# Performance work log

Measured on AMD Instinct MI355X. Metric: run time of the kernel, lower is better.

## Reference

```python
import jax, jax.numpy as jnp
import numpy as np

FEATS = 768
HEAD = 12


def _phi(t):
    # elu feature map + 1 (guarantees positivity)
    return jax.nn.elu(t) + 1.0


def setup_inputs() -> dict:
    key = jax.random.key(0)
    ks = jax.random.split(key, 9)
    f = FEATS
    s = 1.0 / np.sqrt(f)
    x = jax.random.normal(ks[0], (4, 4096, f), dtype=jnp.float32)
    # weights stored as [in, out] so projection is x @ W + b
    Wq = jax.random.normal(ks[1], (f, f), dtype=jnp.float32) * s
    bq = jax.random.normal(ks[2], (f,), dtype=jnp.float32) * 0.01
    Wk = jax.random.normal(ks[3], (f, f), dtype=jnp.float32) * s
    bk = jax.random.normal(ks[4], (f,), dtype=jnp.float32) * 0.01
    Wv = jax.random.normal(ks[5], (f, f), dtype=jnp.float32) * s
    bv = jax.random.normal(ks[6], (f,), dtype=jnp.float32) * 0.01
    Wo = jax.random.normal(ks[7], (f, f), dtype=jnp.float32) * s
    bo = jax.random.normal(ks[8], (f,), dtype=jnp.float32) * 0.01
    return {"x": x, "Wq": Wq, "bq": bq, "Wk": Wk, "bk": bk,
            "Wv": Wv, "bv": bv, "Wo": Wo, "bo": bo}


def reference(x, Wq, bq, Wk, bk, Wv, bv, Wo, bo):
    b, n, f = x.shape
    h = HEAD
    d = f // h
    # project and split heads: [b, h, n, d]
    def heads(t):
        return t.reshape(b, n, h, d).transpose(0, 2, 1, 3)
    q = _phi(heads(x @ Wq + bq))
    k = _phi(heads(x @ Wk + bk))
    v = heads(x @ Wv + bv)
    # kv summary: [b, h, d, d] (sum over sequence)
    kv = jnp.einsum('bhnd,bhne->bhde', k, v)
    # normalizer: z[b,h,l] = 1 / (q[b,h,l,:] . sum_n k[b,h,n,:])  (no eps, as in source)
    ksum = k.sum(axis=2)                      # [b, h, d]
    z = 1.0 / jnp.einsum('bhld,bhd->bhl', q, ksum)  # [b, h, n]
    num = jnp.einsum('bhld,bhde->bhle', q, kv)      # [b, h, n, d]
    normed = num * z[..., None]                     # [b, h, n, d]
    out = normed.transpose(0, 2, 1, 3).reshape(b, n, f)  # [b, n, f]
    return out @ Wo + bo  # dropout p=0.0 -> identity
```

## Files before the change

kernel.cpp:

```cpp
#include <hip/hip_runtime.h>
#include <cstdint>
#include <cstddef>

#define DEVI __device__ __forceinline__

typedef short    shortx8 __attribute__((ext_vector_type(8)));
typedef short    shortx4 __attribute__((ext_vector_type(4)));
typedef short    shortx2 __attribute__((ext_vector_type(2)));
typedef __bf16   bf16x8  __attribute__((ext_vector_type(8)));
typedef float    floatx4 __attribute__((ext_vector_type(4)));

DEVI unsigned short f2b(float f) {
    union { float f; unsigned u; } a; a.f = f;
    unsigned r = a.u + 0x7fffu + ((a.u >> 16) & 1u);
    return (unsigned short)(r >> 16);
}
DEVI float b2f(unsigned short u) {
    union { unsigned u; float f; } a; a.u = ((unsigned)u) << 16;
    return a.f;
}

DEVI floatx4 mfma_bf16(bf16x8 a, bf16x8 b, floatx4 c) {
    return __builtin_amdgcn_mfma_f32_16x16x32_bf16(a, b, c, 0, 0, 0);
}

DEVI void glds16(const ushort* g, ushort* l) {
    __builtin_amdgcn_global_load_lds(
        (const __attribute__((address_space(1))) void*)g,
        (__attribute__((address_space(3))) void*)l, 16, 0, 0);
}

__global__ void k_prep(const float* __restrict__ x, ushort* __restrict__ xb,
                       const float* __restrict__ Wq, const float* __restrict__ Wk,
                       const float* __restrict__ Wv, const float* __restrict__ Wo,
                       ushort* __restrict__ Wt, ushort* __restrict__ Wot,
                       const float* __restrict__ bq, const float* __restrict__ bk,
                       const float* __restrict__ bv, float* __restrict__ bqkv) {
    __shared__ float tile[64][65];
    const int bid = blockIdx.x, t = threadIdx.x;
    if (bid < 6144) {
        size_t i = ((size_t)bid * 256 + t) * 8;
        float4 v0 = *(const float4*)(x + i);
        float4 v1 = *(const float4*)(x + i + 4);
        shortx8 o;
        o[0] = (short)f2b(v0.x); o[1] = (short)f2b(v0.y);
        o[2] = (short)f2b(v0.z); o[3] = (short)f2b(v0.w);
        o[4] = (short)f2b(v1.x); o[5] = (short)f2b(v1.y);
        o[6] = (short)f2b(v1.z); o[7] = (short)f2b(v1.w);
        *(shortx8*)(xb + i) = o;
    } else if (bid < 6720) {
        int pid = bid - 6144;
        int zi = pid / 144, rem = pid % 144;
        const float* W = (zi == 0) ? Wq : (zi == 1) ? Wk : (zi == 2) ? Wv : Wo;
        const int i0 = (rem / 12) * 64, j0 = (rem % 12) * 64;
        const int c = t & 63, r4 = t >> 6;
        for (int rr = r4; rr < 64; rr += 4)
            tile[rr][c] = W[(size_t)(i0 + rr) * 768 + j0 + c];
        __syncthreads();
        ushort* dst = (zi < 3) ? (Wt + (size_t)(zi * 768) * 768) : Wot;
        for (int jj = r4; jj < 64; jj += 4)
            dst[(size_t)(j0 + jj) * 768 + i0 + c] = f2b(tile[c][jj]);
    } else {
        int j = (bid - 6720) * 256 + t;
        if (j < 2304) {
            const float* src = (j < 768) ? bq : (j < 1536) ? bk : bv;
            bqkv[j] = src[j % 768];
        }
    }
}

template <int MODE>
__global__ __launch_bounds__(256, 2) void k_gemm(
    const ushort* __restrict__ A, const ushort* __restrict__ Bt,
    const float* __restrict__ bias, void* __restrict__ Cout, int Ncols) {
    constexpr int K = 768;
    __shared__ ushort As[128 * 64];
    __shared__ ushort Bs[128 * 64];
    const int m0 = blockIdx.x * 128;
    const int n0 = blockIdx.y * 128;
    const int tid = threadIdx.x;
    const int w = tid >> 6, lane = tid & 63;

    const int lr = lane >> 3;
    const int lc = ((lane & 7) ^ lr) * 8;
    const ushort* ag[4]; const ushort* bg[4]; ushort* al[4]; ushort* bl[4];
#pragma unroll
    for (int i = 0; i < 4; ++i) {
        ag[i] = A  + (size_t)(m0 + w * 32 + i * 8 + lr) * K + lc;
        bg[i] = Bt + (size_t)(n0 + w * 32 + i * 8 + lr) * K + lc;
        al[i] = As + (w * 32 + i * 8) * 64;
        bl[i] = Bs + (w * 32 + i * 8) * 64;
    }

    const int rBase = (w >> 1) * 64;
    const int nBase = (w & 1) * 64;
    const int fr = lane & 15;
    const int q4 = lane >> 4;

    floatx4 acc[4][4] = {};

    for (int k0 = 0; k0 < K; k0 += 64) {
#pragma unroll
        for (int i = 0; i < 4; ++i) glds16(ag[i] + k0, al[i]);
#pragma unroll
        for (int i = 0; i < 4; ++i) glds16(bg[i] + k0, bl[i]);
        __syncthreads();
#pragma unroll
        for (int kc = 0; kc < 2; ++kc) {
            const int off = ((kc * 4 + q4) ^ (fr & 7)) * 8;
            bf16x8 af[4], bf[4];
#pragma unroll
            for (int rt = 0; rt < 4; ++rt)
                af[rt] = *(const bf16x8*)(As + (rBase + rt * 16 + fr) * 64 + off);
#pragma unroll
            for (int nt = 0; nt < 4; ++nt)
                bf[nt] = *(const bf16x8*)(Bs + (nBase + nt * 16 + fr) * 64 + off);
#pragma unroll
            for (int rt = 0; rt < 4; ++rt)
#pragma unroll
                for (int nt = 0; nt < 4; ++nt)
                    acc[rt][nt] = mfma_bf16(af[rt], bf[nt], acc[rt][nt]);
        }
        __syncthreads();
    }

#pragma unroll
    for (int rt = 0; rt < 4; ++rt) {
#pragma unroll
        for (int nt = 0; nt < 4; ++nt) {
#pragma unroll
            for (int r = 0; r < 4; ++r) {
                int m = m0 + rBase + rt * 16 + q4 * 4 + r;
                int n = n0 + nBase + nt * 16 + fr;
                float v = acc[rt][nt][r] + bias[n];
                if (MODE == 0) {
                    if (n < 1536) v = (v > 0.f) ? (v + 1.f) : __expf(v);
                    ((ushort*)Cout)[(size_t)m * Ncols + n] = f2b(v);
                } else {
                    ((float*)Cout)[(size_t)m * Ncols + n] = v;
                }
            }
        }
    }
}

__global__ __launch_bounds__(256) void k_kv(const ushort* __restrict__ QKV,
                                            float* __restrict__ kvp) {
    const int bh = blockIdx.x, s = blockIdx.y;
    const int bb = bh / 12, head = bh % 12;
    __shared__ ushort kS[64 * 70];
    __shared__ ushort vS[64 * 70];
    const int t = threadIdx.x, w = t >> 6, lane = t & 63;
    const int fr = lane & 15, fk = (lane >> 4) * 8;

    floatx4 acc[5] = {};
    const int n_ld = t >> 2, c16 = (t & 3) * 16;
    const ushort* base = QKV + (size_t)(bb * 4096 + s * 512) * 2304 + 768 + head * 64 + c16;

    for (int rr = 0; rr < 8; ++rr) {
        if (rr) __syncthreads();
        {
            const ushort* kp = base + (size_t)(rr * 64 + n_ld) * 2304;
            union { shortx8 v8; shortx2 v2[4]; } k0, k1, v0, v1;
            k0.v8 = *(const shortx8*)(kp);
            k1.v8 = *(const shortx8*)(kp + 8);
            v0.v8 = *(const shortx8*)(kp + 768);
            v1.v8 = *(const shortx8*)(kp + 776);
            ushort* kd = kS + n_ld * 70 + c16;
            ushort* vd = vS + n_ld * 70 + c16;
#pragma unroll
            for (int i = 0; i < 4; ++i) {
                *(shortx2*)(kd + 2 * i)     = k0.v2[i];
                *(shortx2*)(kd + 8 + 2 * i) = k1.v2[i];
                *(shortx2*)(vd + 2 * i)     = v0.v2[i];
                *(shortx2*)(vd + 8 + 2 * i) = v1.v2[i];
            }
        }
        __syncthreads();
#pragma unroll
        for (int kl = 0; kl < 64; kl += 32) {
            union { bf16x8 v; ushort u[8]; } bfr, afr[4];
#pragma unroll
            for (int i = 0; i < 8; ++i) {
                int n = kl + fk + i;
                bfr.u[i] = kS[n * 70 + w * 16 + fr];
#pragma unroll
                for (int mt = 0; mt < 4; ++mt)
                    afr[mt].u[i] = vS[n * 70 + mt * 16 + fr];
            }
            union { bf16x8 v; ushort u[8]; } ones;
            ushort ov = (fr == 0) ? (ushort)0x3F80 : (ushort)0;
#pragma unroll
            for (int i = 0; i < 8; ++i) ones.u[i] = ov;
#pragma unroll
            for (int mt = 0; mt < 4; ++mt)
                acc[mt] = mfma_bf16(afr[mt].v, bfr.v, acc[mt]);
            acc[4] = mfma_bf16(ones.v, bfr.v, acc[4]);
        }
    }

    float* dst = kvp + ((size_t)bh * 8 + s) * (65 * 64);
#pragma unroll
    for (int mt = 0; mt < 4; ++mt)
#pragma unroll
        for (int r = 0; r < 4; ++r)
            dst[(mt * 16 + (lane >> 4) * 4 + r) * 64 + w * 16 + fr] = acc[mt][r];
    if (lane < 16) dst[64 * 64 + w * 16 + lane] = acc[4][0];
}

__global__ void k_kvred(const float* __restrict__ kvp, ushort* __restrict__ kvb) {
    int t4 = (blockIdx.x * 256 + threadIdx.x) * 4;
    int bh = t4 / 4160, rem = t4 % 4160;
    const float* p = kvp + (size_t)bh * 8 * 4160 + rem;
    float4 sum = {0.f, 0.f, 0.f, 0.f};
    for (int i = 0; i < 8; ++i) {
        float4 a = *(const float4*)(p + (size_t)i * 4160);
        sum.x += a.x; sum.y += a.y; sum.z += a.z; sum.w += a.w;
    }
    shortx4 o;
    o[0] = (short)f2b(sum.x); o[1] = (short)f2b(sum.y);
    o[2] = (short)f2b(sum.z); o[3] = (short)f2b(sum.w);
    *(shortx4*)(kvb + t4) = o;
}

__global__ __launch_bounds__(256) void k_num(const ushort* __restrict__ QKV,
                                             const ushort* __restrict__ kvb,
                                             ushort* __restrict__ normed) {
    const int bh = blockIdx.x, l0 = blockIdx.y * 128;
    const int bb = bh / 12, head = bh % 12;
    __shared__ ushort qsh[128 * 72];
    __shared__ ushort kvT[80 * 72];
    __shared__ float dnm[128];
    const int t = threadIdx.x, w = t >> 6, lane = t & 63;

    {
        const ushort* kvbb = kvb + (size_t)bh * 4160;
        int c8 = (t & 7) * 8;
        for (int r0 = (t >> 3); r0 < 65; r0 += 32)
            *(shortx8*)(kvT + r0 * 72 + c8) = *(const shortx8*)(kvbb + r0 * 64 + c8);
    }
    for (int idx = t; idx < 15 * 72; idx += 256) kvT[65 * 72 + idx] = 0;

    const ushort* qg = QKV + (size_t)(bb * 4096 + l0) * 2304 + head * 64;
    {
        int row = t >> 3, c8 = (t & 7) * 8;
#pragma unroll
        for (int i = 0; i < 4; ++i) {
            shortx8 v = *(const shortx8*)(qg + (size_t)(i * 32 + row) * 2304 + c8);
            *(shortx8*)(qsh + (i * 32 + row) * 72 + c8) = v;
        }
    }
    __syncthreads();

    const int fr = lane & 15, fk = (lane >> 4) * 8;
    floatx4 acc[2][5] = {};
#pragma unroll
    for (int kc = 0; kc < 2; ++kc) {
        bf16x8 a[2], b[5];
#pragma unroll
        for (int rt = 0; rt < 2; ++rt)
            a[rt] = *(const bf16x8*)(qsh + (w * 32 + rt * 16 + fr) * 72 + kc * 32 + fk);
#pragma unroll
        for (int nt = 0; nt < 5; ++nt)
            b[nt] = *(const bf16x8*)(kvT + (nt * 16 + fr) * 72 + kc * 32 + fk);
#pragma unroll
        for (int rt = 0; rt < 2; ++rt)
#pragma unroll
            for (int nt = 0; nt < 5; ++nt)
                acc[rt][nt] = mfma_bf16(a[rt], b[nt], acc[rt][nt]);
    }
    if (fr == 0) {
#pragma unroll
        for (int rt = 0; rt < 2; ++rt)
#pragma unroll
            for (int r = 0; r < 4; ++r)
                dnm[w * 32 + rt * 16 + (lane >> 4) * 4 + r] = acc[rt][4][r];
    }
    __syncthreads();
#pragma unroll
    for (int rt = 0; rt < 2; ++rt) {
#pragma unroll
        for (int r = 0; r < 4; ++r) {
            int ml = w * 32 + rt * 16 + (lane >> 4) * 4 + r;
            float z = 1.f / dnm[ml];
            size_t base = (size_t)(bb * 4096 + l0 + ml) * 768 + head * 64;
#pragma unroll
            for (int nt = 0; nt < 4; ++nt)
                normed[base + nt * 16 + fr] = f2b(acc[rt][nt][r] * z);
        }
    }
}

extern "C" void kernel_launch(void* const* d_in, const int* in_sizes, int n_in,
                              void* d_out, int out_size, void* d_ws, size_t ws_size,
                              hipStream_t stream) {
    const float* x  = (const float*)d_in[0];
    const float* Wq = (const float*)d_in[1];
    const float* bq = (const float*)d_in[2];
    const float* Wk = (const float*)d_in[3];
    const float* bk = (const float*)d_in[4];
    const float* Wv = (const float*)d_in[5];
    const float* bv = (const float*)d_in[6];
    const float* Wo = (const float*)d_in[7];
    const float* bo = (const float*)d_in[8];

    char* ws = (char*)d_ws;
    ushort* Xb   = (ushort*)(ws);
    ushort* Wt   = (ushort*)(ws + 25165824);
    ushort* Wot  = (ushort*)(ws + 28704768);
    float*  bqkv = (float*)(ws + 29884416);
    ushort* QKV  = (ushort*)(ws + 29893632);
    float*  kvp  = (float*)(ws + 105391104);
    ushort* kvb  = (ushort*)(ws + 111780864);
    ushort* normed = Xb;

    k_prep <<<dim3(6729),      256, 0, stream>>>(x, Xb, Wq, Wk, Wv, Wo, Wt, Wot,
                                                 bq, bk, bv, bqkv);
    k_gemm<0><<<dim3(128, 18), 256, 0, stream>>>(Xb, Wt, bqkv, (void*)QKV, 2304);
    k_kv   <<<dim3(48, 8),     256, 0, stream>>>(QKV, kvp);
    k_kvred<<<dim3(195),       256, 0, stream>>>(kvp, kvb);
    k_num  <<<dim3(48, 32),    256, 0, stream>>>(QKV, kvb, normed);
    k_gemm<1><<<dim3(128, 6),  256, 0, stream>>>(normed, Wot, bo, d_out, 768);
}
```

Measured before the change: 237.8 us.

## Load GEMM B operand directly to registers and stage normed output through LDS

The GEMM kernel stops staging the weight tile in shared memory. Each wave loads its B fragments straight from global memory into registers, which halves LDS use, and launch bounds are raised to three blocks per CU for more occupancy. The attention kernel now writes its normalized output into shared memory first and then stores it to global with coalesced 16-byte writes instead of scattered 2-byte stores. The risks are that the B loads from global are now duplicated across waves and less coalesced, and that register pressure rises under the tighter launch bound.

Result: slower. 313.6 us (+31.8%).

```diff
diff --git a/kernel.cpp b/kernel.cpp
--- a/kernel.cpp
+++ b/kernel.cpp
@@ -70,12 +70,11 @@
 }
 
 template <int MODE>
-__global__ __launch_bounds__(256, 2) void k_gemm(
+__global__ __launch_bounds__(256, 3) void k_gemm(
     const ushort* __restrict__ A, const ushort* __restrict__ Bt,
     const float* __restrict__ bias, void* __restrict__ Cout, int Ncols) {
     constexpr int K = 768;
     __shared__ ushort As[128 * 64];
-    __shared__ ushort Bs[128 * 64];
     const int m0 = blockIdx.x * 128;
     const int n0 = blockIdx.y * 128;
     const int tid = threadIdx.x;
@@ -83,13 +82,11 @@
 
     const int lr = lane >> 3;
     const int lc = ((lane & 7) ^ lr) * 8;
-    const ushort* ag[4]; const ushort* bg[4]; ushort* al[4]; ushort* bl[4];
+    const ushort* ag[4]; ushort* al[4];
 #pragma unroll
     for (int i = 0; i < 4; ++i) {
-        ag[i] = A  + (size_t)(m0 + w * 32 + i * 8 + lr) * K + lc;
-        bg[i] = Bt + (size_t)(n0 + w * 32 + i * 8 + lr) * K + lc;
+        ag[i] = A + (size_t)(m0 + w * 32 + i * 8 + lr) * K + lc;
         al[i] = As + (w * 32 + i * 8) * 64;
-        bl[i] = Bs + (w * 32 + i * 8) * 64;
     }
 
     const int rBase = (w >> 1) * 64;
@@ -97,29 +94,35 @@
     const int fr = lane & 15;
     const int q4 = lane >> 4;
 
+    const ushort* bp[4];
+#pragma unroll
+    for (int nt = 0; nt < 4; ++nt)
+        bp[nt] = Bt + (size_t)(n0 + nBase + nt * 16 + fr) * K + q4 * 8;
+
     floatx4 acc[4][4] = {};
 
     for (int k0 = 0; k0 < K; k0 += 64) {
 #pragma unroll
         for (int i = 0; i < 4; ++i) glds16(ag[i] + k0, al[i]);
-#pragma unroll
-        for (int i = 0; i < 4; ++i) glds16(bg[i] + k0, bl[i]);
+        bf16x8 bf[2][4];
+#pragma unroll
+        for (int kc = 0; kc < 2; ++kc)
+#pragma unroll
+            for (int nt = 0; nt < 4; ++nt)
+                bf[kc][nt] = *(const bf16x8*)(bp[nt] + k0 + kc * 32);
         __syncthreads();
 #pragma unroll
         for (int kc = 0; kc < 2; ++kc) {
             const int off = ((kc * 4 + q4) ^ (fr & 7)) * 8;
-            bf16x8 af[4], bf[4];
+            bf16x8 af[4];
 #pragma unroll
             for (int rt = 0; rt < 4; ++rt)
                 af[rt] = *(const bf16x8*)(As + (rBase + rt * 16 + fr) * 64 + off);
 #pragma unroll
-            for (int nt = 0; nt < 4; ++nt)
-                bf[nt] = *(const bf16x8*)(Bs + (nBase + nt * 16 + fr) * 64 + off);
-#pragma unroll
             for (int rt = 0; rt < 4; ++rt)
 #pragma unroll
                 for (int nt = 0; nt < 4; ++nt)
-                    acc[rt][nt] = mfma_bf16(af[rt], bf[nt], acc[rt][nt]);
+                    acc[rt][nt] = mfma_bf16(af[rt], bf[kc][nt], acc[rt][nt]);
         }
         __syncthreads();
     }
@@ -277,16 +280,27 @@
                 dnm[w * 32 + rt * 16 + (lane >> 4) * 4 + r] = acc[rt][4][r];
     }
     __syncthreads();
+
+    ushort* osh = qsh;
 #pragma unroll
     for (int rt = 0; rt < 2; ++rt) {
 #pragma unroll
         for (int r = 0; r < 4; ++r) {
             int ml = w * 32 + rt * 16 + (lane >> 4) * 4 + r;
             float z = 1.f / dnm[ml];
-            size_t base = (size_t)(bb * 4096 + l0 + ml) * 768 + head * 64;
 #pragma unroll
             for (int nt = 0; nt < 4; ++nt)
-                normed[base + nt * 16 + fr] = f2b(acc[rt][nt][r] * z);
+                osh[ml * 72 + nt * 16 + fr] = f2b(acc[rt][nt][r] * z);
+        }
+    }
+    __syncthreads();
+    {
+        int row = t >> 3, c8 = (t & 7) * 8;
+#pragma unroll
+        for (int i = 0; i < 4; ++i) {
+            int r2 = i * 32 + row;
+            *(shortx8*)(normed + (size_t)(bb * 4096 + l0 + r2) * 768 + head * 64 + c8) =
+                *(const shortx8*)(osh + r2 * 72 + c8);
         }
     }
 }
```

## Fuse numerator/normalization into output projection GEMM per head

Applied to the files above, without the earlier changes.

Removes the separate k_num kernel and the normed intermediate buffer by computing q·kv and the normalizer per head inside the output-projection GEMM block, then feeding the normalized bf16 tile straight from shared memory into the Wo MFMA loop. kvred now writes a padded 72-column, zero-filled layout so the fused kernel can copy it into LDS directly. This drops a global write and read of the normalized activations and one launch. In exchange, each of the 6 column blocks recomputes the q·kv product for its rows (6x redundant small MFMA work) and adds extra syncs per head.

New measurement: 271.3 us. +14.1%, slower.

```diff
diff --git a/kernel.cpp b/kernel.cpp
--- a/kernel.cpp
+++ b/kernel.cpp
@@ -69,10 +69,9 @@
     }
 }
 
-template <int MODE>
-__global__ __launch_bounds__(256, 2) void k_gemm(
+__global__ __launch_bounds__(256, 2) void k_qkv(
     const ushort* __restrict__ A, const ushort* __restrict__ Bt,
-    const float* __restrict__ bias, void* __restrict__ Cout, int Ncols) {
+    const float* __restrict__ bias, ushort* __restrict__ Cout) {
     constexpr int K = 768;
     __shared__ ushort As[128 * 64];
     __shared__ ushort Bs[128 * 64];
@@ -83,7 +82,8 @@
 
     const int lr = lane >> 3;
     const int lc = ((lane & 7) ^ lr) * 8;
-    const ushort* ag[4]; const ushort* bg[4]; ushort* al[4]; ushort* bl[4];
+    const ushort* ag[4]; ushort* al[4];
+    const ushort* bg[4]; ushort* bl[4];
 #pragma unroll
     for (int i = 0; i < 4; ++i) {
         ag[i] = A  + (size_t)(m0 + w * 32 + i * 8 + lr) * K + lc;
@@ -133,12 +133,8 @@
                 int m = m0 + rBase + rt * 16 + q4 * 4 + r;
                 int n = n0 + nBase + nt * 16 + fr;
                 float v = acc[rt][nt][r] + bias[n];
-                if (MODE == 0) {
-                    if (n < 1536) v = (v > 0.f) ? (v + 1.f) : __expf(v);
-                    ((ushort*)Cout)[(size_t)m * Ncols + n] = f2b(v);
-                } else {
-                    ((float*)Cout)[(size_t)m * Ncols + n] = v;
-                }
+                if (n < 1536) v = (v > 0.f) ? (v + 1.f) : __expf(v);
+                Cout[(size_t)m * 2304 + n] = f2b(v);
             }
         }
     }
@@ -210,83 +206,124 @@
 
 __global__ void k_kvred(const float* __restrict__ kvp, ushort* __restrict__ kvb) {
     int t4 = (blockIdx.x * 256 + threadIdx.x) * 4;
-    int bh = t4 / 4160, rem = t4 % 4160;
-    const float* p = kvp + (size_t)bh * 8 * 4160 + rem;
-    float4 sum = {0.f, 0.f, 0.f, 0.f};
-    for (int i = 0; i < 8; ++i) {
-        float4 a = *(const float4*)(p + (size_t)i * 4160);
-        sum.x += a.x; sum.y += a.y; sum.z += a.z; sum.w += a.w;
-    }
-    shortx4 o;
-    o[0] = (short)f2b(sum.x); o[1] = (short)f2b(sum.y);
-    o[2] = (short)f2b(sum.z); o[3] = (short)f2b(sum.w);
+    int bh = t4 / 5760, rem = t4 % 5760;
+    int r = rem / 72, c = rem % 72;
+    shortx4 o = {0, 0, 0, 0};
+    if (r < 65 && c < 64) {
+        const float* p = kvp + (size_t)bh * 8 * 4160 + r * 64 + c;
+        float4 sum = {0.f, 0.f, 0.f, 0.f};
+        for (int s = 0; s < 8; ++s) {
+            float4 a = *(const float4*)(p + (size_t)s * 4160);
+            sum.x += a.x; sum.y += a.y; sum.z += a.z; sum.w += a.w;
+        }
+        o[0] = (short)f2b(sum.x); o[1] = (short)f2b(sum.y);
+        o[2] = (short)f2b(sum.z); o[3] = (short)f2b(sum.w);
+    }
     *(shortx4*)(kvb + t4) = o;
 }
 
-__global__ __launch_bounds__(256) void k_num(const ushort* __restrict__ QKV,
-                                             const ushort* __restrict__ kvb,
-                                             ushort* __restrict__ normed) {
-    const int bh = blockIdx.x, l0 = blockIdx.y * 128;
-    const int bb = bh / 12, head = bh % 12;
-    __shared__ ushort qsh[128 * 72];
+__global__ __launch_bounds__(256, 2) void k_out(
+    const ushort* __restrict__ QKV, const ushort* __restrict__ kvb,
+    const ushort* __restrict__ Wot, const float* __restrict__ bo,
+    float* __restrict__ Out) {
+    __shared__ ushort Qs[128 * 64];
+    __shared__ ushort Bs[128 * 64];
     __shared__ ushort kvT[80 * 72];
-    __shared__ float dnm[128];
+    const int m0 = blockIdx.x * 128;
+    const int n0 = blockIdx.y * 128;
+    const int bb = m0 >> 12;
     const int t = threadIdx.x, w = t >> 6, lane = t & 63;
-
-    {
-        const ushort* kvbb = kvb + (size_t)bh * 4160;
-        int c8 = (t & 7) * 8;
-        for (int r0 = (t >> 3); r0 < 65; r0 += 32)
-            *(shortx8*)(kvT + r0 * 72 + c8) = *(const shortx8*)(kvbb + r0 * 64 + c8);
-    }
-    for (int idx = t; idx < 15 * 72; idx += 256) kvT[65 * 72 + idx] = 0;
-
-    const ushort* qg = QKV + (size_t)(bb * 4096 + l0) * 2304 + head * 64;
-    {
-        int row = t >> 3, c8 = (t & 7) * 8;
-#pragma unroll
-        for (int i = 0; i < 4; ++i) {
-            shortx8 v = *(const shortx8*)(qg + (size_t)(i * 32 + row) * 2304 + c8);
-            *(shortx8*)(qsh + (i * 32 + row) * 72 + c8) = v;
-        }
-    }
-    __syncthreads();
-
-    const int fr = lane & 15, fk = (lane >> 4) * 8;
-    floatx4 acc[2][5] = {};
-#pragma unroll
-    for (int kc = 0; kc < 2; ++kc) {
-        bf16x8 a[2], b[5];
-#pragma unroll
-        for (int rt = 0; rt < 2; ++rt)
-            a[rt] = *(const bf16x8*)(qsh + (w * 32 + rt * 16 + fr) * 72 + kc * 32 + fk);
-#pragma unroll
-        for (int nt = 0; nt < 5; ++nt)
-            b[nt] = *(const bf16x8*)(kvT + (nt * 16 + fr) * 72 + kc * 32 + fk);
-#pragma unroll
-        for (int rt = 0; rt < 2; ++rt)
+    const int lr = lane >> 3, lc = ((lane & 7) ^ lr) * 8;
+    const int fr = lane & 15, q4 = lane >> 4, fk = q4 * 8;
+    const int rB2 = w * 32;
+    const int rBase = (w >> 1) * 64, nBase = (w & 1) * 64;
+
+    const ushort* qg[4]; ushort* ql[4]; const ushort* wg[4]; ushort* bl[4];
+#pragma unroll
+    for (int i = 0; i < 4; ++i) {
+        qg[i] = QKV + (size_t)(m0 + w * 32 + i * 8 + lr) * 2304 + lc;
+        wg[i] = Wot + (size_t)(n0 + w * 32 + i * 8 + lr) * 768 + lc;
+        ql[i] = Qs + (w * 32 + i * 8) * 64;
+        bl[i] = Bs + (w * 32 + i * 8) * 64;
+    }
+
+    floatx4 acc[4][4] = {};
+
+    for (int h = 0; h < 12; ++h) {
+        __syncthreads();
+#pragma unroll
+        for (int i = 0; i < 4; ++i) glds16(qg[i] + h * 64, ql[i]);
+#pragma unroll
+        for (int i = 0; i < 4; ++i) glds16(wg[i] + h * 64, bl[i]);
+        {
+            const ushort* kvg = kvb + (size_t)(bb * 12 + h) * 5760;
+            for (int idx = t; idx < 720; idx += 256)
+                *(shortx8*)(kvT + idx * 8) = *(const shortx8*)(kvg + idx * 8);
+        }
+        __syncthreads();
+
+        floatx4 a2[2][5] = {};
+#pragma unroll
+        for (int kc = 0; kc < 2; ++kc) {
+            const int off = ((kc * 4 + q4) ^ (fr & 7)) * 8;
+            bf16x8 qa[2], kb[5];
+#pragma unroll
+            for (int rt = 0; rt < 2; ++rt)
+                qa[rt] = *(const bf16x8*)(Qs + (rB2 + rt * 16 + fr) * 64 + off);
 #pragma unroll
             for (int nt = 0; nt < 5; ++nt)
-                acc[rt][nt] = mfma_bf16(a[rt], b[nt], acc[rt][nt]);
-    }
-    if (fr == 0) {
-#pragma unroll
-        for (int rt = 0; rt < 2; ++rt)
-#pragma unroll
-            for (int r = 0; r < 4; ++r)
-                dnm[w * 32 + rt * 16 + (lane >> 4) * 4 + r] = acc[rt][4][r];
-    }
-    __syncthreads();
-#pragma unroll
-    for (int rt = 0; rt < 2; ++rt) {
-#pragma unroll
-        for (int r = 0; r < 4; ++r) {
-            int ml = w * 32 + rt * 16 + (lane >> 4) * 4 + r;
-            float z = 1.f / dnm[ml];
-            size_t base = (size_t)(bb * 4096 + l0 + ml) * 768 + head * 64;
+                kb[nt] = *(const bf16x8*)(kvT + (nt * 16 + fr) * 72 + kc * 32 + fk);
+#pragma unroll
+            for (int rt = 0; rt < 2; ++rt)
+#pragma unroll
+                for (int nt = 0; nt < 5; ++nt)
+                    a2[rt][nt] = mfma_bf16(qa[rt], kb[nt], a2[rt][nt]);
+        }
+#pragma unroll
+        for (int rt = 0; rt < 2; ++rt) {
+#pragma unroll
+            for (int r = 0; r < 4; ++r) {
+                float den = __shfl(a2[rt][4][r], lane & 48);
+                float z = 1.f / den;
+                int row = rB2 + rt * 16 + q4 * 4 + r;
+#pragma unroll
+                for (int nt = 0; nt < 4; ++nt) {
+                    int e = nt * 16 + fr;
+                    Qs[row * 64 + (((e >> 3) ^ (row & 7)) * 8) + (e & 7)] =
+                        f2b(a2[rt][nt][r] * z);
+                }
+            }
+        }
+        __syncthreads();
+
+#pragma unroll
+        for (int kc = 0; kc < 2; ++kc) {
+            const int off = ((kc * 4 + q4) ^ (fr & 7)) * 8;
+            bf16x8 af[4], bf[4];
+#pragma unroll
+            for (int rt = 0; rt < 4; ++rt)
+                af[rt] = *(const bf16x8*)(Qs + (rBase + rt * 16 + fr) * 64 + off);
 #pragma unroll
             for (int nt = 0; nt < 4; ++nt)
-                normed[base + nt * 16 + fr] = f2b(acc[rt][nt][r] * z);
+                bf[nt] = *(const bf16x8*)(Bs + (nBase + nt * 16 + fr) * 64 + off);
+#pragma unroll
+            for (int rt = 0; rt < 4; ++rt)
+#pragma unroll
+                for (int nt = 0; nt < 4; ++nt)
+                    acc[rt][nt] = mfma_bf16(af[rt], bf[nt], acc[rt][nt]);
+        }
+    }
+
+#pragma unroll
+    for (int rt = 0; rt < 4; ++rt) {
+#pragma unroll
+        for (int nt = 0; nt < 4; ++nt) {
+#pragma unroll
+            for (int r = 0; r < 4; ++r) {
+                int m = m0 + rBase + rt * 16 + q4 * 4 + r;
+                int n = n0 + nBase + nt * 16 + fr;
+                Out[(size_t)m * 768 + n] = acc[rt][nt][r] + bo[n];
+            }
         }
     }
 }
@@ -312,13 +349,11 @@
     ushort* QKV  = (ushort*)(ws + 29893632);
     float*  kvp  = (float*)(ws + 105391104);
     ushort* kvb  = (ushort*)(ws + 111780864);
-    ushort* normed = Xb;
-
-    k_prep <<<dim3(6729),      256, 0, stream>>>(x, Xb, Wq, Wk, Wv, Wo, Wt, Wot,
-                                                 bq, bk, bv, bqkv);
-    k_gemm<0><<<dim3(128, 18), 256, 0, stream>>>(Xb, Wt, bqkv, (void*)QKV, 2304);
-    k_kv   <<<dim3(48, 8),     256, 0, stream>>>(QKV, kvp);
-    k_kvred<<<dim3(195),       256, 0, stream>>>(kvp, kvb);
-    k_num  <<<dim3(48, 32),    256, 0, stream>>>(QKV, kvb, normed);
-    k_gemm<1><<<dim3(128, 6),  256, 0, stream>>>(normed, Wot, bo, d_out, 768);
-}
+
+    k_prep <<<dim3(6729),     256, 0, stream>>>(x, Xb, Wq, Wk, Wv, Wo, Wt, Wot,
+                                                bq, bk, bv, bqkv);
+    k_qkv  <<<dim3(128, 18),  256, 0, stream>>>(Xb, Wt, bqkv, QKV);
+    k_kv   <<<dim3(48, 8),    256, 0, stream>>>(QKV, kvp);
+    k_kvred<<<dim3(270),      256, 0, stream>>>(kvp, kvb);
+    k_out  <<<dim3(128, 6),   256, 0, stream>>>(QKV, kvb, Wot, bo, (float*)d_out);
+}
```
